# Performance work log

Measured on AMD Instinct MI355X. Metric: run time of the kernel, lower is better.

## Reference

```python
import jax, jax.numpy as jnp
import numpy as np

M = 20000   # users
N = 20000   # items
E = 320000  # edges per channel per direction
C = 4       # channels
H = 4       # attention heads
D_IN = 256
D_OUT = 128
NEG_SLOPE = 0.01  # F.leaky_relu default


def setup_inputs() -> dict:
    key = jax.random.key(0)
    ks = jax.random.split(key, 12)
    u_prev = jax.random.normal(ks[0], (M, D_IN), jnp.float32)
    i_prev = jax.random.normal(ks[1], (N, D_IN), jnp.float32)
    # raw (pre-cumsum) shared parameters, 0.1*randn as in the module
    w_user = 0.1 * jax.random.normal(ks[2], (C, D_IN, D_OUT), jnp.float32)
    w_item = 0.1 * jax.random.normal(ks[3], (C, D_IN, D_OUT), jnp.float32)
    a_u_src = 0.1 * jax.random.normal(ks[4], (H, C, D_OUT), jnp.float32)
    a_u_dst = 0.1 * jax.random.normal(ks[5], (H, C, D_OUT), jnp.float32)
    a_i_src = 0.1 * jax.random.normal(ks[6], (H, C, D_OUT), jnp.float32)
    a_i_dst = 0.1 * jax.random.normal(ks[7], (H, C, D_OUT), jnp.float32)
    u2i_row = jax.random.randint(ks[8], (C, E), 0, M, jnp.int32)
    u2i_col = jax.random.randint(ks[9], (C, E), 0, N, jnp.int32)
    i2u_row = jax.random.randint(ks[10], (C, E), 0, N, jnp.int32)
    i2u_col = jax.random.randint(ks[11], (C, E), 0, M, jnp.int32)
    return dict(u_prev=u_prev, i_prev=i_prev, w_user=w_user, w_item=w_item,
                a_u_src=a_u_src, a_u_dst=a_u_dst, a_i_src=a_i_src, a_i_dst=a_i_dst,
                u2i_row=u2i_row, u2i_col=u2i_col, i2u_row=i2u_row, i2u_col=i2u_col)


def _segment_softmax(logits, seg, num_segments):
    # neighborhood softmax over edges grouped by destination row
    mx = jax.ops.segment_max(logits, seg, num_segments=num_segments)
    ex = jnp.exp(logits - mx[seg])
    den = jax.ops.segment_sum(ex, seg, num_segments=num_segments)
    return ex / den[seg]


def _attend(row, col, h_src, h_dst, a_src, a_dst, n_rows):
    # a_src, a_dst: (H, D_OUT). reduce_att = sum over heads; inner nonlinear = identity.
    # Node-level scores first (equivalent to gathering then dotting, much cheaper).
    s_src = h_src @ a_src.T  # (m, H)
    s_dst = h_dst @ a_dst.T  # (n, H)
    out = jnp.zeros((n_rows, h_dst.shape[1]), h_dst.dtype)
    for j in range(a_src.shape[0]):  # fixed small head loop
        logits = jax.nn.leaky_relu(s_src[row, j] + s_dst[col, j], NEG_SLOPE)  # (E,)
        att = _segment_softmax(logits, row, n_rows)                            # (E,)
        # sparse-dense matmul: out[r] += att_e * h_dst[c]
        out = out + jax.ops.segment_sum(att[:, None] * h_dst[col], row, num_segments=n_rows)
    return out


def reference(u_prev, i_prev, w_user, w_item, a_u_src, a_u_dst, a_i_src, a_i_dst,
              u2i_row, u2i_col, i2u_row, i2u_col):
    # SharedParameter[idx] = sum(xs[:idx+1]) -> cumulative sum along channel axis
    Wu = jnp.cumsum(w_user, axis=0)   # (C, D_IN, D_OUT)
    Wi = jnp.cumsum(w_item, axis=0)
    Aus = jnp.cumsum(a_u_src, axis=1)  # (H, C, D_OUT)
    Aud = jnp.cumsum(a_u_dst, axis=1)
    Ais = jnp.cumsum(a_i_src, axis=1)
    Aid = jnp.cumsum(a_i_dst, axis=1)

    u_outs, i_outs = [], []
    for c in range(C):
        u = u_prev @ Wu[c]  # (M, D_OUT), bias = 0 in MCGATLayer
        i = i_prev @ Wi[c]  # (N, D_OUT)
        u_next = _attend(u2i_row[c], u2i_col[c], u, i, Aus[:, c], Aud[:, c], M)
        i_next = _attend(i2u_row[c], i2u_col[c], i, u, Ais[:, c], Aid[:, c], N)
        u_outs.append(u_next)
        i_outs.append(i_next)

    # reduce_chnl == 'cat' (uniq_i = all nodes -> index_copy is identity placement)
    u_final = jax.nn.relu(jnp.concatenate(u_outs, axis=1))  # (M, C*D_OUT)
    i_final = jax.nn.relu(jnp.concatenate(i_outs, axis=1))  # (N, C*D_OUT)
    return (u_final, i_final)
```

## Files before the change

kernel.cpp:

```cpp
#include <hip/hip_runtime.h>
#include <math.h>

#define M_NODES 20000
#define MPAD    20096
#define NE      320000
#define NC      4
#define NH      4
#define DIN     256
#define DOUT    128
#define DCAT    512

#define RPB   256
#define NBKT  79
#define EPB   2048
#define NBLK  157
#define CAP   8192

typedef __attribute__((ext_vector_type(8))) _Float16 half8v;
typedef __attribute__((ext_vector_type(2))) _Float16 half2v;
typedef __attribute__((ext_vector_type(4))) float f32x4;

__device__ __forceinline__ unsigned short f2h(float x) {
    _Float16 h = (_Float16)x;
    return __builtin_bit_cast(unsigned short, h);
}
__device__ __forceinline__ void gload16(const void* g, void* l) {
    __builtin_amdgcn_global_load_lds(
        (const __attribute__((address_space(1))) void*)g,
        (__attribute__((address_space(3))) void*)l,
        16, 0, 0);
}

__global__ __launch_bounds__(256) void k_prep(const float* __restrict__ u_prev, const float* __restrict__ i_prev,
                                              const float* __restrict__ w_user, const float* __restrict__ w_item,
                                              const float* __restrict__ a_u_src, const float* __restrict__ a_u_dst,
                                              const float* __restrict__ a_i_src, const float* __restrict__ a_i_dst,
                                              const int* __restrict__ u2i_row, const int* __restrict__ i2u_row,
                                              unsigned short* __restrict__ AbU, unsigned short* __restrict__ AbI,
                                              unsigned short* __restrict__ BTu, unsigned short* __restrict__ BTi,
                                              unsigned short* __restrict__ Bscore, int* __restrict__ cnt3) {
    __shared__ int hist[NBKT];
    int bid = blockIdx.x, tid = threadIdx.x;
    if (bid < 5000) {
        int sideI = bid >= 2500;
        int t = (sideI ? bid - 2500 : bid) * 256 + tid;
        int row = t >> 5, kc = (t & 31) * 8;
        const float* src = sideI ? i_prev : u_prev;
        unsigned short* dst = sideI ? AbI : AbU;
        float4 x0 = *(const float4*)(src + (size_t)row * DIN + kc);
        float4 x1 = *(const float4*)(src + (size_t)row * DIN + kc + 4);
        float xs[8] = {x0.x, x0.y, x0.z, x0.w, x1.x, x1.y, x1.z, x1.w};
        unsigned int H[4];
#pragma unroll
        for (int p = 0; p < 4; ++p)
            H[p] = (unsigned int)f2h(xs[2 * p]) | ((unsigned int)f2h(xs[2 * p + 1]) << 16);
        *(uint4*)(dst + (size_t)row * 256 + kc) = make_uint4(H[0], H[1], H[2], H[3]);
        return;
    }
    if (bid < 6256) {
        int sub = bid - 5000;
        int combo = sub / NBLK, blk = sub % NBLK;
        int c = combo >> 1, dir = combo & 1;
        const int* rows = (dir ? i2u_row : u2i_row) + (size_t)c * NE;
        if (tid < NBKT) hist[tid] = 0;
        __syncthreads();
        int e0 = blk * EPB + tid * 8;
        if (e0 + 8 <= NE) {
            int4 r0 = *(const int4*)(rows + e0);
            int4 r1 = *(const int4*)(rows + e0 + 4);
            atomicAdd(&hist[r0.x >> 8], 1); atomicAdd(&hist[r0.y >> 8], 1);
            atomicAdd(&hist[r0.z >> 8], 1); atomicAdd(&hist[r0.w >> 8], 1);
            atomicAdd(&hist[r1.x >> 8], 1); atomicAdd(&hist[r1.y >> 8], 1);
            atomicAdd(&hist[r1.z >> 8], 1); atomicAdd(&hist[r1.w >> 8], 1);
        }
        __syncthreads();
        if (tid < NBKT) cnt3[((size_t)combo * NBKT + tid) * NBLK + blk] = hist[tid];
        return;
    }
    if (bid < 6384) {
        int idx = (bid - 6256) * 256 + tid;
        int k = idx >> 7, j = idx & 127;
        float su = 0.f, si = 0.f;
        for (int c = 0; c < NC; ++c) {
            su += w_user[((size_t)c * DIN + k) * DOUT + j];
            si += w_item[((size_t)c * DIN + k) * DOUT + j];
            size_t n = (size_t)(c * DOUT + j) * 256;
            BTu[n + k] = f2h(su);
            BTi[n + k] = f2h(si);
        }
        return;
    }
    {
        int t = (bid - 6384) * 256 + tid;
        int side = t >> 11, nt = (t >> 10) & 1, kstep = (t >> 6) & 15, ln = t & 63;
        int g = ln >> 4, l15 = ln & 15;
        int cc = nt * 2 + (l15 >> 3), kind = (l15 >> 2) & 1, h = l15 & 3;
        const float* araw = kind ? (side ? a_u_dst : a_i_dst) : (side ? a_i_src : a_u_src);
        unsigned int out2[4];
#pragma unroll
        for (int p = 0; p < 4; ++p) {
            unsigned short e2[2];
#pragma unroll
            for (int q = 0; q < 2; ++q) {
                int j = p * 2 + q;
                int k = kstep * 32 + g * 8 + j;
                int kc = k >> 7, d = k & 127;
                float s = 0.f;
                if (kc == cc)
                    for (int c2 = 0; c2 <= cc; ++c2) s += araw[(h * NC + c2) * DOUT + d];
                e2[q] = f2h(s);
            }
            out2[p] = (unsigned int)e2[0] | ((unsigned int)e2[1] << 16);
        }
        *(uint4*)(Bscore + ((size_t)(((side * 2 + nt) * 16 + kstep) * 64 + ln)) * 8) =
            make_uint4(out2[0], out2[1], out2[2], out2[3]);
    }
}

__global__ __launch_bounds__(256) void k_gmm(const unsigned short* __restrict__ AbU,
                                             const unsigned short* __restrict__ AbI,
                                             const unsigned short* __restrict__ BTu,
                                             const unsigned short* __restrict__ BTi,
                                             unsigned short* __restrict__ fbu,
                                             unsigned short* __restrict__ fbi,
                                             int* __restrict__ cnt3, int* __restrict__ btot,
                                             int* __restrict__ bbase) {
    __shared__ unsigned short As[128 * 64];
    __shared__ unsigned short Bs[128 * 64];
    __shared__ int tot[128];
    int bid = blockIdx.x, tid = threadIdx.x;
    if (bid < 1256) {
        int side = bid >= 628;
        int t = side ? bid - 628 : bid;
        int c = t / 157, mb = t % 157;
        const unsigned short* Ab = side ? AbI : AbU;
        const unsigned short* BT = side ? BTi : BTu;
        unsigned short* fb       = side ? fbi : fbu;
        int m0 = mb * 128;
        int w = tid >> 6, lane = tid & 63;
        int wrb = (w >> 1) * 64, wcb = (w & 1) * 64;
        int l15 = lane & 15, g = lane >> 4;
        int srow = lane >> 3, scol = (lane & 7) * 8;
        f32x4 acc[4][4] = {};
        for (int kt = 0; kt < 4; ++kt) {
            int k0 = kt * 64;
#pragma unroll
            for (int tt = 0; tt < 4; ++tt) {
                int chunk = w * 4 + tt;
                int row8 = chunk * 8 + srow;
                gload16(Ab + (size_t)(m0 + row8) * 256 + k0 + scol, (char*)As + chunk * 1024);
                gload16(BT + (size_t)(c * 128 + row8) * 256 + k0 + scol, (char*)Bs + chunk * 1024);
            }
            __syncthreads();
#pragma unroll
            for (int ks = 0; ks < 2; ++ks) {
                half8v a[4], b[4];
#pragma unroll
                for (int i = 0; i < 4; ++i)
                    a[i] = *(const half8v*)(&As[(wrb + i * 16 + l15) * 64 + ks * 32 + g * 8]);
#pragma unroll
                for (int j = 0; j < 4; ++j)
                    b[j] = *(const half8v*)(&Bs[(wcb + j * 16 + l15) * 64 + ks * 32 + g * 8]);
#pragma unroll
                for (int i = 0; i < 4; ++i)
#pragma unroll
                    for (int j = 0; j < 4; ++j)
                        acc[i][j] = __builtin_amdgcn_mfma_f32_16x16x32_f16(a[i], b[j], acc[i][j], 0, 0, 0);
            }
            __syncthreads();
        }
#pragma unroll
        for (int i = 0; i < 4; ++i) {
#pragma unroll
            for (int r = 0; r < 4; ++r) {
                int node = m0 + wrb + i * 16 + g * 4 + r;
                if (node < M_NODES) {
#pragma unroll
                    for (int j = 0; j < 4; ++j) {
                        int d = wcb + j * 16 + l15;
                        fb[((size_t)c * M_NODES + node) * DOUT + d] = f2h(acc[i][j][r]);
                    }
                }
            }
        }
        return;
    }
    {
        int combo = bid - 1256;
        if (tid < NBKT) {
            size_t base = ((size_t)combo * NBKT + tid) * NBLK;
            int run = 0;
            for (int b = 0; b < NBLK; ++b) {
                int v = cnt3[base + b];
                cnt3[base + b] = run;
                run += v;
            }
            tot[tid] = run;
            btot[combo * NBKT + tid] = run;
        }
        __syncthreads();
        if (tid < 64) {
            int carry = 0;
            for (int ch = 0; ch < 2; ++ch) {
                int idx = ch * 64 + tid;
                int v = (idx < NBKT) ? tot[idx] : 0;
                int inc = v;
                for (int o = 1; o < 64; o <<= 1) {
                    int tv = __shfl_up(inc, o);
                    if (tid >= o) inc += tv;
                }
                if (idx < NBKT) bbase[combo * NBKT + idx] = carry + inc - v;
                carry += __shfl(inc, 63);
            }
        }
    }
}

__global__ __launch_bounds__(256) void k_sb(const unsigned short* __restrict__ fbu,
                                            const unsigned short* __restrict__ fbi,
                                            const unsigned short* __restrict__ Bscore,
                                            float* __restrict__ su_src, float* __restrict__ su_dst,
                                            float* __restrict__ si_src, float* __restrict__ si_dst,
                                            const int* __restrict__ u2i_row, const int* __restrict__ u2i_col,
                                            const int* __restrict__ i2u_row, const int* __restrict__ i2u_col,
                                            const int* __restrict__ cnt3, const int* __restrict__ bbase,
                                            unsigned int* __restrict__ pairbuf) {
    __shared__ int cur[NBKT];
    int bid = blockIdx.x, tid = threadIdx.x;
    if (bid < 626) {
        int side = bid >= 313;
        int bx = side ? bid - 313 : bid;
        const unsigned short* fb = side ? fbi : fbu;
        int wv = tid >> 6, lane = tid & 63;
        int nb = (bx * 4 + wv) * 16;
        int l15 = lane & 15, g = lane >> 4;
        int node = nb + l15;
        int nload = node < M_NODES ? node : 0;
        f32x4 acc0 = {}, acc1 = {};
        const unsigned short* bs = Bscore + (size_t)side * 2 * 16 * 64 * 8;
        for (int ks = 0; ks < 16; ++ks) {
            int cch = ks >> 2;
            int off = (ks & 3) * 32 + g * 8;
            half8v a  = *(const half8v*)(fb + ((size_t)cch * M_NODES + nload) * DOUT + off);
            half8v b0 = *(const half8v*)(bs + ((size_t)(ks) * 64 + lane) * 8);
            half8v b1 = *(const half8v*)(bs + ((size_t)(16 + ks) * 64 + lane) * 8);
            acc0 = __builtin_amdgcn_mfma_f32_16x16x32_f16(a, b0, acc0, 0, 0, 0);
            acc1 = __builtin_amdgcn_mfma_f32_16x16x32_f16(a, b1, acc1, 0, 0, 0);
        }
        int kind = (l15 >> 2) & 1, h = l15 & 3;
        float* dst = kind ? (side ? si_dst : su_dst) : (side ? si_src : su_src);
#pragma unroll
        for (int nt = 0; nt < 2; ++nt) {
            int cc = nt * 2 + (l15 >> 3);
            f32x4 acc = nt ? acc1 : acc0;
#pragma unroll
            for (int rr = 0; rr < 4; ++rr) {
                int nrow = nb + g * 4 + rr;
                if (nrow < M_NODES)
                    dst[((size_t)cc * M_NODES + nrow) * 4 + h] = acc[rr];
            }
        }
        return;
    }
    {
        int sub = bid - 626;
        int combo = sub / NBLK, blk = sub % NBLK;
        int c = combo >> 1, dir = combo & 1;
        const int* rows = (dir ? i2u_row : u2i_row) + (size_t)c * NE;
        const int* cols = (dir ? i2u_col : u2i_col) + (size_t)c * NE;
        if (tid < NBKT)
            cur[tid] = bbase[combo * NBKT + tid] + cnt3[((size_t)combo * NBKT + tid) * NBLK + blk];
        __syncthreads();
        unsigned int* pb = pairbuf + (size_t)combo * NE;
        int e0 = blk * EPB + tid * 8;
        if (e0 + 8 <= NE) {
            int4 r0 = *(const int4*)(rows + e0);
            int4 r1 = *(const int4*)(rows + e0 + 4);
            int4 c0 = *(const int4*)(cols + e0);
            int4 c1 = *(const int4*)(cols + e0 + 4);
            int rr[8] = {r0.x, r0.y, r0.z, r0.w, r1.x, r1.y, r1.z, r1.w};
            int cc[8] = {c0.x, c0.y, c0.z, c0.w, c1.x, c1.y, c1.z, c1.w};
#pragma unroll
            for (int k = 0; k < 8; ++k) {
                int pos = atomicAdd(&cur[rr[k] >> 8], 1);
                pb[pos] = ((unsigned int)rr[k] << 16) | (unsigned int)cc[k];
            }
        }
    }
}

__global__ __launch_bounds__(256) void k_finalize(const unsigned int* __restrict__ pairbuf,
                                                  const int* __restrict__ bbase, const int* __restrict__ btot,
                                                  int* __restrict__ csroff, int* __restrict__ csrcol) {
    __shared__ int hist[RPB];
    __shared__ int cur[RPB];
    __shared__ int lcol[CAP];
    int tid = threadIdx.x, bkt = blockIdx.x, combo = blockIdx.y;
    int base = bbase[combo * NBKT + bkt];
    int cntb = btot[combo * NBKT + bkt];
    const unsigned int* pb = pairbuf + (size_t)combo * NE + base;
    int* ccol = csrcol + (size_t)combo * NE + base;
    hist[tid] = 0;
    __syncthreads();
    for (int k = tid; k < cntb; k += 256)
        atomicAdd(&hist[(pb[k] >> 16) & (RPB - 1)], 1);
    __syncthreads();
    for (int st = 1; st < RPB; st <<= 1) {
        int v = (tid >= st) ? hist[tid - st] : 0;
        __syncthreads();
        hist[tid] += v;
        __syncthreads();
    }
    int ex = (tid == 0) ? 0 : hist[tid - 1];
    cur[tid] = ex;
    int row = bkt * RPB + tid;
    if (row < M_NODES) csroff[combo * (M_NODES + 1) + row] = base + ex;
    if (bkt == NBKT - 1 && tid == 0) csroff[combo * (M_NODES + 1) + M_NODES] = NE;
    __syncthreads();
    for (int k = tid; k < cntb; k += 256) {
        unsigned int p = pb[k];
        int rl  = (p >> 16) & (RPB - 1);
        int col = (int)(p & 0xffffu);
        int pos = atomicAdd(&cur[rl], 1);
        if (pos < CAP) lcol[pos] = col; else ccol[pos] = col;
    }
    __syncthreads();
    int lim = min(cntb, CAP);
    for (int k = tid; k < lim; k += 256) ccol[k] = lcol[k];
}

__device__ void attend_row_wave(int r, int s0, int deg, const float* __restrict__ ssrc,
                                const float* __restrict__ sdst, const unsigned short* __restrict__ fbd,
                                const int* __restrict__ co, float* __restrict__ o, int lane) {
    if (deg <= 64) {
        float w = 0.f;
        int cl = 0;
        if (deg > 0) {
            float4 ssv = *(const float4*)(ssrc + (size_t)r * 4);
            float ss[4] = {ssv.x, ssv.y, ssv.z, ssv.w};
            float lg[4];
            if (lane < deg) {
                cl = co[s0 + lane];
                float4 sdv = *(const float4*)(sdst + (size_t)cl * 4);
                float sd[4] = {sdv.x, sdv.y, sdv.z, sdv.w};
#pragma unroll
                for (int h = 0; h < 4; ++h) {
                    float x = ss[h] + sd[h];
                    lg[h] = x > 0.f ? x : 0.01f * x;
                }
            } else {
#pragma unroll
                for (int h = 0; h < 4; ++h) lg[h] = -1e30f;
            }
            float ex[4], den[4];
#pragma unroll
            for (int h = 0; h < 4; ++h) {
                ex[h] = __expf(fminf(lg[h], 80.f));
                den[h] = ex[h];
            }
#pragma unroll
            for (int h = 0; h < 4; ++h)
                for (int o2 = 32; o2; o2 >>= 1) den[h] += __shfl_xor(den[h], o2);
#pragma unroll
            for (int h = 0; h < 4; ++h) w += ex[h] * (1.f / den[h]);
        }
        int q = lane >> 4, l16 = lane & 15;
        const unsigned short* fbl = fbd + l16 * 8;
        float a8[8] = {};
        for (int j = 0; j < deg; j += 4) {
            int e = j + q;
            float we = __shfl(w, e & 63);
            int   ce = __shfl(cl, e & 63);
            if (e < deg) {
                half8v v = *(const half8v*)(fbl + (size_t)ce * DOUT);
#pragma unroll
                for (int k = 0; k < 8; ++k) a8[k] = fmaf(we, (float)v[k], a8[k]);
            }
        }
#pragma unroll
        for (int i = 0; i < 8; ++i) {
            a8[i] += __shfl_xor(a8[i], 16);
            a8[i] += __shfl_xor(a8[i], 32);
        }
        if (lane < 16) {
            float4 r0 = make_float4(fmaxf(a8[0], 0.f), fmaxf(a8[1], 0.f), fmaxf(a8[2], 0.f), fmaxf(a8[3], 0.f));
            float4 r1 = make_float4(fmaxf(a8[4], 0.f), fmaxf(a8[5], 0.f), fmaxf(a8[6], 0.f), fmaxf(a8[7], 0.f));
            *(float4*)(o + l16 * 8) = r0;
            *(float4*)(o + l16 * 8 + 4) = r1;
        }
        return;
    }
    float acc0 = 0.f, acc1 = 0.f;
    {
        float4 ssv = *(const float4*)(ssrc + (size_t)r * 4);
        float ss[4] = {ssv.x, ssv.y, ssv.z, ssv.w};
        float den[4] = {0.f, 0.f, 0.f, 0.f};
        for (int base = 0; base < deg; base += 64) {
            int e = base + lane;
            float ex[4] = {0.f, 0.f, 0.f, 0.f};
            if (e < deg) {
                int cl = co[s0 + e];
                float4 sdv = *(const float4*)(sdst + (size_t)cl * 4);
                float sd[4] = {sdv.x, sdv.y, sdv.z, sdv.w};
#pragma unroll
                for (int h = 0; h < 4; ++h) {
                    float x = ss[h] + sd[h];
                    x = x > 0.f ? x : 0.01f * x;
                    ex[h] = __expf(fminf(x, 80.f));
                }
            }
#pragma unroll
            for (int h = 0; h < 4; ++h) {
                float v = ex[h];
                for (int o2 = 32; o2; o2 >>= 1) v += __shfl_xor(v, o2);
                den[h] += v;
            }
        }
        float inv[4];
#pragma unroll
        for (int h = 0; h < 4; ++h) inv[h] = 1.f / den[h];
        for (int base = 0; base < deg; base += 64) {
            int e = base + lane;
            float w = 0.f;
            int cl = 0;
            if (e < deg) {
                cl = co[s0 + e];
                float4 sdv = *(const float4*)(sdst + (size_t)cl * 4);
                float sd[4] = {sdv.x, sdv.y, sdv.z, sdv.w};
#pragma unroll
                for (int h = 0; h < 4; ++h) {
                    float x = ss[h] + sd[h];
                    x = x > 0.f ? x : 0.01f * x;
                    w += __expf(fminf(x, 80.f)) * inv[h];
                }
            }
            int cnt2 = min(64, deg - base);
            for (int j = 0; j < cnt2; ++j) {
                float wj = __shfl(w, j);
                int   cj = __shfl(cl, j);
                half2v hv = *(const half2v*)(fbd + (size_t)cj * DOUT + lane * 2);
                acc0 = fmaf(wj, (float)hv[0], acc0);
                acc1 = fmaf(wj, (float)hv[1], acc1);
            }
        }
    }
    o[lane * 2]     = fmaxf(acc0, 0.f);
    o[lane * 2 + 1] = fmaxf(acc1, 0.f);
}

__global__ __launch_bounds__(256) void k_attend(const unsigned short* __restrict__ fbu, const unsigned short* __restrict__ fbi,
                                                const float* __restrict__ su_src, const float* __restrict__ su_dst,
                                                const float* __restrict__ si_src, const float* __restrict__ si_dst,
                                                const int* __restrict__ off, const int* __restrict__ cols,
                                                float* __restrict__ out) {
    int bid = blockIdx.x;
    int combo = bid & 7, c = combo >> 1, dir = combo & 1;
    int wavein = threadIdx.x >> 6, lane = threadIdx.x & 63;
    int half = lane >> 5, l = lane & 31;
    int rbase = (bid >> 3) * 8 + wavein * 2;
    const float* ssrc = (dir ? si_src : su_src) + (size_t)c * M_NODES * NH;
    const float* sdst = (dir ? su_dst : si_dst) + (size_t)c * M_NODES * NH;
    const unsigned short* fbd = (dir ? fbu : fbi) + (size_t)c * M_NODES * DOUT;
    const int* co = cols + (size_t)combo * NE;
    const int* offc = off + combo * (M_NODES + 1);
    int r = rbase + half;
    int s0 = offc[r];
    int deg = offc[r + 1] - s0;
    int degmax = max(deg, __shfl_xor(deg, 32));
    float* o = out + ((size_t)(dir ? M_NODES + r : r)) * DCAT + c * DOUT;

    if (degmax <= 32) {
        float w = 0.f;
        int cl = 0;
        if (deg > 0) {
            float4 ssv = *(const float4*)(ssrc + (size_t)r * 4);
            float ss[4] = {ssv.x, ssv.y, ssv.z, ssv.w};
            float lg[4];
            if (l < deg) {
                cl = co[s0 + l];
                float4 sdv = *(const float4*)(sdst + (size_t)cl * 4);
                float sd[4] = {sdv.x, sdv.y, sdv.z, sdv.w};
#pragma unroll
                for (int h = 0; h < 4; ++h) {
                    float x = ss[h] + sd[h];
                    lg[h] = x > 0.f ? x : 0.01f * x;
                }
            } else {
#pragma unroll
                for (int h = 0; h < 4; ++h) lg[h] = -1e30f;
            }
            float ex[4], den[4];
#pragma unroll
            for (int h = 0; h < 4; ++h) {
                ex[h] = __expf(fminf(lg[h], 80.f));
                den[h] = ex[h];
            }
#pragma unroll
            for (int h = 0; h < 4; ++h)
                for (int o2 = 16; o2; o2 >>= 1) den[h] += __shfl_xor(den[h], o2);
#pragma unroll
            for (int h = 0; h < 4; ++h) w += ex[h] * (1.f / den[h]);
        }
        int q2 = (l >> 4), l16 = l & 15;
        const unsigned short* fbl = fbd + l16 * 8;
        float a8[8] = {};
        int hb = half * 32;
        int j = 0;
        for (; j + 8 <= deg; j += 8) {
            int e0 = j + q2, e1 = j + 2 + q2, e2 = j + 4 + q2, e3 = j + 6 + q2;
            float w0 = __shfl(w, hb + e0), w1 = __shfl(w, hb + e1);
            float w2 = __shfl(w, hb + e2), w3 = __shfl(w, hb + e3);
            int   c0 = __shfl(cl, hb + e0), c1 = __shfl(cl, hb + e1);
            int   c2 = __shfl(cl, hb + e2), c3 = __shfl(cl, hb + e3);
            half8v v0 = *(const half8v*)(fbl + (size_t)c0 * DOUT);
            half8v v1 = *(const half8v*)(fbl + (size_t)c1 * DOUT);
            half8v v2 = *(const half8v*)(fbl + (size_t)c2 * DOUT);
            half8v v3 = *(const half8v*)(fbl + (size_t)c3 * DOUT);
#pragma unroll
            for (int k = 0; k < 8; ++k) a8[k] = fmaf(w0, (float)v0[k], a8[k]);
#pragma unroll
            for (int k = 0; k < 8; ++k) a8[k] = fmaf(w1, (float)v1[k], a8[k]);
#pragma unroll
            for (int k = 0; k < 8; ++k) a8[k] = fmaf(w2, (float)v2[k], a8[k]);
#pragma unroll
            for (int k = 0; k < 8; ++k) a8[k] = fmaf(w3, (float)v3[k], a8[k]);
        }
        for (; j < deg; j += 4) {
            int e0 = j + q2, e1 = j + 2 + q2;
            float w0 = __shfl(w, hb + min(e0, 31));
            float w1 = __shfl(w, hb + min(e1, 31));
            int   c0 = __shfl(cl, hb + min(e0, 31));
            int   c1 = __shfl(cl, hb + min(e1, 31));
            w0 = (e0 < deg) ? w0 : 0.f;
            w1 = (e1 < deg) ? w1 : 0.f;
            half8v v0 = *(const half8v*)(fbl + (size_t)c0 * DOUT);
            half8v v1 = *(const half8v*)(fbl + (size_t)c1 * DOUT);
#pragma unroll
            for (int k = 0; k < 8; ++k) a8[k] = fmaf(w0, (float)v0[k], a8[k]);
#pragma unroll
            for (int k = 0; k < 8; ++k) a8[k] = fmaf(w1, (float)v1[k], a8[k]);
        }
#pragma unroll
        for (int i = 0; i < 8; ++i) a8[i] += __shfl_xor(a8[i], 16);
        if (l < 16) {
            float4 r0 = make_float4(fmaxf(a8[0], 0.f), fmaxf(a8[1], 0.f), fmaxf(a8[2], 0.f), fmaxf(a8[3], 0.f));
            float4 r1 = make_float4(fmaxf(a8[4], 0.f), fmaxf(a8[5], 0.f), fmaxf(a8[6], 0.f), fmaxf(a8[7], 0.f));
            *(float4*)(o + l16 * 8) = r0;
            *(float4*)(o + l16 * 8 + 4) = r1;
        }
        return;
    }

    for (int rr = 0; rr < 2; ++rr) {
        int r2 = rbase + rr;
        int t0 = offc[r2];
        int d2 = offc[r2 + 1] - t0;
        float* o2 = out + ((size_t)(dir ? M_NODES + r2 : r2)) * DCAT + c * DOUT;
        attend_row_wave(r2, t0, d2, ssrc, sdst, fbd, co, o2, lane);
    }
}

extern "C" void kernel_launch(void* const* d_in, const int* in_sizes, int n_in,
                              void* d_out, int out_size, void* d_ws, size_t ws_size,
                              hipStream_t stream) {
    const float* u_prev  = (const float*)d_in[0];
    const float* i_prev  = (const float*)d_in[1];
    const float* w_user  = (const float*)d_in[2];
    const float* w_item  = (const float*)d_in[3];
    const float* a_u_src = (const float*)d_in[4];
    const float* a_u_dst = (const float*)d_in[5];
    const float* a_i_src = (const float*)d_in[6];
    const float* a_i_dst = (const float*)d_in[7];
    const int* u2i_row = (const int*)d_in[8];
    const int* u2i_col = (const int*)d_in[9];
    const int* i2u_row = (const int*)d_in[10];
    const int* i2u_col = (const int*)d_in[11];
    float* out = (float*)d_out;

    char* ws = (char*)d_ws;
    size_t woff = 0;
    auto alloc = [&](size_t bytes) -> char* {
        char* p = ws + woff;
        woff += (bytes + 255) & ~(size_t)255;
        return p;
    };
    unsigned short* AbU   = (unsigned short*)alloc((size_t)MPAD * 256 * 2);
    unsigned short* AbI   = (unsigned short*)alloc((size_t)MPAD * 256 * 2);
    unsigned short* BTu   = (unsigned short*)alloc((size_t)512 * 256 * 2);
    unsigned short* BTi   = (unsigned short*)alloc((size_t)512 * 256 * 2);
    unsigned short* Bscore= (unsigned short*)alloc((size_t)2 * 2 * 16 * 64 * 8 * 2);
    unsigned short* fbu   = (unsigned short*)alloc((size_t)NC * M_NODES * DOUT * 2);
    unsigned short* fbi   = (unsigned short*)alloc((size_t)NC * M_NODES * DOUT * 2);
    float* su_src = (float*)alloc((size_t)NC * M_NODES * NH * 4);
    float* su_dst = (float*)alloc((size_t)NC * M_NODES * NH * 4);
    float* si_src = (float*)alloc((size_t)NC * M_NODES * NH * 4);
    float* si_dst = (float*)alloc((size_t)NC * M_NODES * NH * 4);
    int* csroff   = (int*)alloc((size_t)8 * (M_NODES + 1) * 4);
    int* csrcol   = (int*)alloc((size_t)8 * NE * 4);
    int* cnt3     = (int*)alloc((size_t)8 * NBKT * NBLK * 4);
    int* btot     = (int*)alloc((size_t)8 * NBKT * 4);
    int* bbase    = (int*)alloc((size_t)8 * NBKT * 4);
    unsigned int* pairbuf = (unsigned int*)alloc((size_t)8 * NE * 4);

    k_prep<<<6400, 256, 0, stream>>>(u_prev, i_prev, w_user, w_item,
                                     a_u_src, a_u_dst, a_i_src, a_i_dst,
                                     u2i_row, i2u_row,
                                     AbU, AbI, BTu, BTi, Bscore, cnt3);
    k_gmm<<<1264, 256, 0, stream>>>(AbU, AbI, BTu, BTi, fbu, fbi, cnt3, btot, bbase);
    k_sb<<<626 + 1256, 256, 0, stream>>>(fbu, fbi, Bscore, su_src, su_dst, si_src, si_dst,
                                         u2i_row, u2i_col, i2u_row, i2u_col,
                                         cnt3, bbase, pairbuf);
    k_finalize<<<dim3(NBKT, 8), 256, 0, stream>>>(pairbuf, bbase, btot, csroff, csrcol);
    k_attend<<<dim3(M_NODES * 8 / 8), 256, 0, stream>>>(fbu, fbi, su_src, su_dst,
                                                        si_src, si_dst, csroff, csrcol, out);
}
```

Measured before the change: 151.8 us.

## Fuse node attention-score MFMA into GEMM epilogue via LDS-staged tile

The GEMM epilogue now also writes its fp16 output tile into shared memory. It then runs a small MFMA against per-channel attention vectors to produce the src/dst node scores directly, so fb no longer has to be re-read from global memory in a separate score kernel. The score vector layout is rebuilt per channel instead of across all channels, and the edge bucket-fill now runs as its own kernel. The cost is a longer GEMM epilogue with an extra barrier and LDS traffic, and the fill work no longer shares a launch with the score work.

```diff
diff --git a/kernel.cpp b/kernel.cpp
--- a/kernel.cpp
+++ b/kernel.cpp
@@ -38,7 +38,7 @@
                                               const int* __restrict__ u2i_row, const int* __restrict__ i2u_row,
                                               unsigned short* __restrict__ AbU, unsigned short* __restrict__ AbI,
                                               unsigned short* __restrict__ BTu, unsigned short* __restrict__ BTi,
-                                              unsigned short* __restrict__ Bscore, int* __restrict__ cnt3) {
+                                              unsigned short* __restrict__ Bvec, int* __restrict__ cnt3) {
     __shared__ int hist[NBKT];
     int bid = blockIdx.x, tid = threadIdx.x;
     if (bid < 5000) {
@@ -92,9 +92,9 @@
     }
     {
         int t = (bid - 6384) * 256 + tid;
-        int side = t >> 11, nt = (t >> 10) & 1, kstep = (t >> 6) & 15, ln = t & 63;
-        int g = ln >> 4, l15 = ln & 15;
-        int cc = nt * 2 + (l15 >> 3), kind = (l15 >> 2) & 1, h = l15 & 3;
+        int lane = t & 63, ks = (t >> 6) & 3, c = (t >> 8) & 3, side = t >> 10;
+        int col = lane & 15, g = lane >> 4;
+        int kind = (col >> 2) & 1, h = col & 3;
         const float* araw = kind ? (side ? a_u_dst : a_i_dst) : (side ? a_i_src : a_u_src);
         unsigned int out2[4];
 #pragma unroll
@@ -103,16 +103,15 @@
 #pragma unroll
             for (int q = 0; q < 2; ++q) {
                 int j = p * 2 + q;
-                int k = kstep * 32 + g * 8 + j;
-                int kc = k >> 7, d = k & 127;
+                int kdim = ks * 32 + g * 8 + j;
                 float s = 0.f;
-                if (kc == cc)
-                    for (int c2 = 0; c2 <= cc; ++c2) s += araw[(h * NC + c2) * DOUT + d];
+                if (col < 8)
+                    for (int c2 = 0; c2 <= c; ++c2) s += araw[(h * NC + c2) * DOUT + kdim];
                 e2[q] = f2h(s);
             }
             out2[p] = (unsigned int)e2[0] | ((unsigned int)e2[1] << 16);
         }
-        *(uint4*)(Bscore + ((size_t)(((side * 2 + nt) * 16 + kstep) * 64 + ln)) * 8) =
+        *(uint4*)(Bvec + ((size_t)(((side * 4 + c) * 4 + ks) * 64 + lane)) * 8) =
             make_uint4(out2[0], out2[1], out2[2], out2[3]);
     }
 }
@@ -121,8 +120,11 @@
                                              const unsigned short* __restrict__ AbI,
                                              const unsigned short* __restrict__ BTu,
                                              const unsigned short* __restrict__ BTi,
+                                             const unsigned short* __restrict__ Bvec,
                                              unsigned short* __restrict__ fbu,
                                              unsigned short* __restrict__ fbi,
+                                             float* __restrict__ su_src, float* __restrict__ su_dst,
+                                             float* __restrict__ si_src, float* __restrict__ si_dst,
                                              int* __restrict__ cnt3, int* __restrict__ btot,
                                              int* __restrict__ bbase) {
     __shared__ unsigned short As[128 * 64];
@@ -173,12 +175,45 @@
         for (int i = 0; i < 4; ++i) {
 #pragma unroll
             for (int r = 0; r < 4; ++r) {
-                int node = m0 + wrb + i * 16 + g * 4 + r;
-                if (node < M_NODES) {
-#pragma unroll
-                    for (int j = 0; j < 4; ++j) {
-                        int d = wcb + j * 16 + l15;
-                        fb[((size_t)c * M_NODES + node) * DOUT + d] = f2h(acc[i][j][r]);
+                int nl = wrb + i * 16 + g * 4 + r;
+                int node = m0 + nl;
+                bool valid = node < M_NODES;
+#pragma unroll
+                for (int j = 0; j < 4; ++j) {
+                    int d = wcb + j * 16 + l15;
+                    unsigned short hv = f2h(acc[i][j][r]);
+                    if (valid) fb[((size_t)c * M_NODES + node) * DOUT + d] = hv;
+                    if (d < 64) As[nl * 64 + d] = hv;
+                    else        Bs[nl * 64 + (d - 64)] = hv;
+                }
+            }
+        }
+        __syncthreads();
+        {
+            half8v bv[4];
+#pragma unroll
+            for (int ks = 0; ks < 4; ++ks)
+                bv[ks] = *(const half8v*)(Bvec + ((size_t)(((side * 4 + c) * 4 + ks) * 64 + lane)) * 8);
+#pragma unroll
+            for (int mt2 = 0; mt2 < 2; ++mt2) {
+                int mt = w * 2 + mt2;
+                f32x4 sacc = {};
+#pragma unroll
+                for (int ks = 0; ks < 4; ++ks) {
+                    int nl = mt * 16 + l15;
+                    const unsigned short* base = (ks < 2) ? As : Bs;
+                    half8v a = *(const half8v*)(&base[nl * 64 + (ks & 1) * 32 + g * 8]);
+                    sacc = __builtin_amdgcn_mfma_f32_16x16x32_f16(a, bv[ks], sacc, 0, 0, 0);
+                }
+                int col = l15;
+                if (col < 8) {
+                    int kind = col >> 2, h = col & 3;
+                    float* dst = kind ? (side ? si_dst : su_dst) : (side ? si_src : su_src);
+#pragma unroll
+                    for (int r = 0; r < 4; ++r) {
+                        int node = m0 + mt * 16 + g * 4 + r;
+                        if (node < M_NODES)
+                            dst[((size_t)c * M_NODES + node) * 4 + h] = sacc[r];
                     }
                 }
             }
@@ -216,75 +251,32 @@
     }
 }
 
-__global__ __launch_bounds__(256) void k_sb(const unsigned short* __restrict__ fbu,
-                                            const unsigned short* __restrict__ fbi,
-                                            const unsigned short* __restrict__ Bscore,
-                                            float* __restrict__ su_src, float* __restrict__ su_dst,
-                                            float* __restrict__ si_src, float* __restrict__ si_dst,
-                                            const int* __restrict__ u2i_row, const int* __restrict__ u2i_col,
-                                            const int* __restrict__ i2u_row, const int* __restrict__ i2u_col,
-                                            const int* __restrict__ cnt3, const int* __restrict__ bbase,
-                                            unsigned int* __restrict__ pairbuf) {
+__global__ __launch_bounds__(256) void k_bfill(const int* __restrict__ u2i_row, const int* __restrict__ u2i_col,
+                                               const int* __restrict__ i2u_row, const int* __restrict__ i2u_col,
+                                               const int* __restrict__ cnt3, const int* __restrict__ bbase,
+                                               unsigned int* __restrict__ pairbuf) {
     __shared__ int cur[NBKT];
     int bid = blockIdx.x, tid = threadIdx.x;
-    if (bid < 626) {
-        int side = bid >= 313;
-        int bx = side ? bid - 313 : bid;
-        const unsigned short* fb = side ? fbi : fbu;
-        int wv = tid >> 6, lane = tid & 63;
-        int nb = (bx * 4 + wv) * 16;
-        int l15 = lane & 15, g = lane >> 4;
-        int node = nb + l15;
-        int nload = node < M_NODES ? node : 0;
-        f32x4 acc0 = {}, acc1 = {};
-        const unsigned short* bs = Bscore + (size_t)side * 2 * 16 * 64 * 8;
-        for (int ks = 0; ks < 16; ++ks) {
-            int cch = ks >> 2;
-            int off = (ks & 3) * 32 + g * 8;
-            half8v a  = *(const half8v*)(fb + ((size_t)cch * M_NODES + nload) * DOUT + off);
-            half8v b0 = *(const half8v*)(bs + ((size_t)(ks) * 64 + lane) * 8);
-            half8v b1 = *(const half8v*)(bs + ((size_t)(16 + ks) * 64 + lane) * 8);
-            acc0 = __builtin_amdgcn_mfma_f32_16x16x32_f16(a, b0, acc0, 0, 0, 0);
-            acc1 = __builtin_amdgcn_mfma_f32_16x16x32_f16(a, b1, acc1, 0, 0, 0);
-        }
-        int kind = (l15 >> 2) & 1, h = l15 & 3;
-        float* dst = kind ? (side ? si_dst : su_dst) : (side ? si_src : su_src);
-#pragma unroll
-        for (int nt = 0; nt < 2; ++nt) {
-            int cc = nt * 2 + (l15 >> 3);
-            f32x4 acc = nt ? acc1 : acc0;
-#pragma unroll
-            for (int rr = 0; rr < 4; ++rr) {
-                int nrow = nb + g * 4 + rr;
-                if (nrow < M_NODES)
-                    dst[((size_t)cc * M_NODES + nrow) * 4 + h] = acc[rr];
-            }
-        }
-        return;
-    }
-    {
-        int sub = bid - 626;
-        int combo = sub / NBLK, blk = sub % NBLK;
-        int c = combo >> 1, dir = combo & 1;
-        const int* rows = (dir ? i2u_row : u2i_row) + (size_t)c * NE;
-        const int* cols = (dir ? i2u_col : u2i_col) + (size_t)c * NE;
-        if (tid < NBKT)
-            cur[tid] = bbase[combo * NBKT + tid] + cnt3[((size_t)combo * NBKT + tid) * NBLK + blk];
-        __syncthreads();
-        unsigned int* pb = pairbuf + (size_t)combo * NE;
-        int e0 = blk * EPB + tid * 8;
-        if (e0 + 8 <= NE) {
-            int4 r0 = *(const int4*)(rows + e0);
-            int4 r1 = *(const int4*)(rows + e0 + 4);
-            int4 c0 = *(const int4*)(cols + e0);
-            int4 c1 = *(const int4*)(cols + e0 + 4);
-            int rr[8] = {r0.x, r0.y, r0.z, r0.w, r1.x, r1.y, r1.z, r1.w};
-            int cc[8] = {c0.x, c0.y, c0.z, c0.w, c1.x, c1.y, c1.z, c1.w};
-#pragma unroll
-            for (int k = 0; k < 8; ++k) {
-                int pos = atomicAdd(&cur[rr[k] >> 8], 1);
-                pb[pos] = ((unsigned int)rr[k] << 16) | (unsigned int)cc[k];
-            }
+    int combo = bid / NBLK, blk = bid % NBLK;
+    int c = combo >> 1, dir = combo & 1;
+    const int* rows = (dir ? i2u_row : u2i_row) + (size_t)c * NE;
+    const int* cols = (dir ? i2u_col : u2i_col) + (size_t)c * NE;
+    if (tid < NBKT)
+        cur[tid] = bbase[combo * NBKT + tid] + cnt3[((size_t)combo * NBKT + tid) * NBLK + blk];
+    __syncthreads();
+    unsigned int* pb = pairbuf + (size_t)combo * NE;
+    int e0 = blk * EPB + tid * 8;
+    if (e0 + 8 <= NE) {
+        int4 r0 = *(const int4*)(rows + e0);
+        int4 r1 = *(const int4*)(rows + e0 + 4);
+        int4 c0 = *(const int4*)(cols + e0);
+        int4 c1 = *(const int4*)(cols + e0 + 4);
+        int rr[8] = {r0.x, r0.y, r0.z, r0.w, r1.x, r1.y, r1.z, r1.w};
+        int cc[8] = {c0.x, c0.y, c0.z, c0.w, c1.x, c1.y, c1.z, c1.w};
+#pragma unroll
+        for (int k = 0; k < 8; ++k) {
+            int pos = atomicAdd(&cur[rr[k] >> 8], 1);
+            pb[pos] = ((unsigned int)rr[k] << 16) | (unsigned int)cc[k];
         }
     }
 }
@@ -588,7 +580,7 @@
     unsigned short* AbI   = (unsigned short*)alloc((size_t)MPAD * 256 * 2);
     unsigned short* BTu   = (unsigned short*)alloc((size_t)512 * 256 * 2);
     unsigned short* BTi   = (unsigned short*)alloc((size_t)512 * 256 * 2);
-    unsigned short* Bscore= (unsigned short*)alloc((size_t)2 * 2 * 16 * 64 * 8 * 2);
+    unsigned short* Bvec  = (unsigned short*)alloc((size_t)2 * 4 * 4 * 64 * 8 * 2);
     unsigned short* fbu   = (unsigned short*)alloc((size_t)NC * M_NODES * DOUT * 2);
     unsigned short* fbi   = (unsigned short*)alloc((size_t)NC * M_NODES * DOUT * 2);
     float* su_src = (float*)alloc((size_t)NC * M_NODES * NH * 4);
@@ -602,14 +594,15 @@
     int* bbase    = (int*)alloc((size_t)8 * NBKT * 4);
     unsigned int* pairbuf = (unsigned int*)alloc((size_t)8 * NE * 4);
 
-    k_prep<<<6400, 256, 0, stream>>>(u_prev, i_prev, w_user, w_item,
+    k_prep<<<6392, 256, 0, stream>>>(u_prev, i_prev, w_user, w_item,
                                      a_u_src, a_u_dst, a_i_src, a_i_dst,
                                      u2i_row, i2u_row,
-                                     AbU, AbI, BTu, BTi, Bscore, cnt3);
-    k_gmm<<<1264, 256, 0, stream>>>(AbU, AbI, BTu, BTi, fbu, fbi, cnt3, btot, bbase);
-    k_sb<<<626 + 1256, 256, 0, stream>>>(fbu, fbi, Bscore, su_src, su_dst, si_src, si_dst,
-                                         u2i_row, u2i_col, i2u_row, i2u_col,
-                                         cnt3, bbase, pairbuf);
+                                     AbU, AbI, BTu, BTi, Bvec, cnt3);
+    k_gmm<<<1264, 256, 0, stream>>>(AbU, AbI, BTu, BTi, Bvec, fbu, fbi,
+                                    su_src, su_dst, si_src, si_dst,
+                                    cnt3, btot, bbase);
+    k_bfill<<<1256, 256, 0, stream>>>(u2i_row, u2i_col, i2u_row, i2u_col,
+                                      cnt3, bbase, pairbuf);
     k_finalize<<<dim3(NBKT, 8), 256, 0, stream>>>(pairbuf, bbase, btot, csroff, csrcol);
     k_attend<<<dim3(M_NODES * 8 / 8), 256, 0, stream>>>(fbu, fbi, su_src, su_dst,
                                                         si_src, si_dst, csroff, csrcol, out);
```

After: 145.3 us. -4.3%, faster.
